# Optimization experiments

Hardware: AMD Instinct MI355X
Metric: run time of the kernel (lower is better)

Reference implementation:

```python
import jax, jax.numpy as jnp
import numpy as np

B, S1, S2 = 4, 2048, 2048
IN1, IN2 = 512, 512
KD, VD, H = 64, 64, 8


def setup_inputs() -> dict:
    key = jax.random.key(0)
    ks = jax.random.split(key, 7)
    x1 = jax.random.normal(ks[0], (B, S1, IN1), dtype=jnp.float32)
    x2 = jax.random.normal(ks[1], (B, S2, IN2), dtype=jnp.float32)
    # nn.Linear weights stored as [out, in]; kaiming-uniform-ish scale
    Wq = jax.random.normal(ks[2], (KD * H, IN1), dtype=jnp.float32) * (1.0 / np.sqrt(IN1))
    Wk = jax.random.normal(ks[3], (KD * H, IN2), dtype=jnp.float32) * (1.0 / np.sqrt(IN2))
    Wv = jax.random.normal(ks[4], (VD * H, IN2), dtype=jnp.float32) * (1.0 / np.sqrt(IN2))
    Wo = jax.random.normal(ks[5], (IN1, VD * H), dtype=jnp.float32) * (1.0 / np.sqrt(VD * H))
    bo = jax.random.normal(ks[6], (IN1,), dtype=jnp.float32) * 0.01
    return {"x1": x1, "x2": x2, "Wq": Wq, "Wk": Wk, "Wv": Wv, "Wo": Wo, "bo": bo}


def reference(x1, x2, Wq, Wk, Wv, Wo, bo):
    b, s1, _ = x1.shape
    s2 = x2.shape[1]
    # projections -> [B, H, S, D]
    q = (x1 @ Wq.T).reshape(b, s1, H, KD).transpose(0, 2, 1, 3)
    k = (x2 @ Wk.T).reshape(b, s2, H, KD).transpose(0, 2, 1, 3)
    v = (x2 @ Wv.T).reshape(b, s2, H, VD).transpose(0, 2, 1, 3)
    # scores [B, H, S1, S2]
    attn = jnp.einsum('bhqd,bhkd->bhqk', q, k) / jnp.sqrt(jnp.float32(KD))
    attn = jax.nn.softmax(attn, axis=-1)
    out = jnp.einsum('bhqk,bhkd->bhqd', attn, v)  # [B, H, S1, VD]
    out = out.transpose(0, 2, 1, 3).reshape(b, s1, H * VD)
    return out @ Wo.T + bo
```

## Files before the change

kernel.cpp:

```cpp
#include <hip/hip_runtime.h>
#include <stdint.h>

typedef __bf16 bf16;
typedef __bf16 bf16x8 __attribute__((ext_vector_type(8)));
typedef __bf16 bf16x4 __attribute__((ext_vector_type(4)));
typedef float f32x4 __attribute__((ext_vector_type(4)));

#define MFMA16x16x32(A, B, C) __builtin_amdgcn_mfma_f32_16x16x32_bf16((A), (B), (C), 0, 0, 0)

__device__ __forceinline__ void gload_lds16(const void* g, void* l) {
  __builtin_amdgcn_global_load_lds((const __attribute__((address_space(1))) void*)g,
                                   (__attribute__((address_space(3))) void*)l,
                                   16, 0, 0);
}

__device__ __forceinline__ float fexp2(float x) { return __builtin_amdgcn_exp2f(x); }

__device__ __forceinline__ bf16x8 cvt8(float4 a, float4 b) {
  bf16x8 o;
  o[0] = (bf16)a.x; o[1] = (bf16)a.y; o[2] = (bf16)a.z; o[3] = (bf16)a.w;
  o[4] = (bf16)b.x; o[5] = (bf16)b.y; o[6] = (bf16)b.z; o[7] = (bf16)b.w;
  return o;
}

__global__ void cast_x(const float* __restrict__ x1, const float* __restrict__ x2,
                       bf16* __restrict__ out) {
  const size_t i = ((size_t)blockIdx.x * blockDim.x + threadIdx.x) * 8;
  const float* src = (i < 4194304) ? x1 + i : x2 + (i - 4194304);
  float4 a = *reinterpret_cast<const float4*>(src);
  float4 b = *reinterpret_cast<const float4*>(src + 4);
  *reinterpret_cast<bf16x8*>(out + i) = cvt8(a, b);
}

template <int MODE>
__global__ __launch_bounds__(256, 4) void proj_kernel(
    const bf16* __restrict__ A0, const bf16* __restrict__ A1,
    const float* __restrict__ W0, const float* __restrict__ W1,
    const float* __restrict__ W2, void* __restrict__ C0, void* __restrict__ C1,
    void* __restrict__ C2, const float* __restrict__ bias) {
  __shared__ bf16 As[2][128 * 32];
  __shared__ bf16 Bs[2][64 * 32];
  const int tid = threadIdx.x;
  const int w = tid >> 6, l = tid & 63;
  const int wr = w >> 1, wc = w & 1;
  const int lr = l & 15, lg = l >> 4;
  const int bm = blockIdx.x, bn = blockIdx.y;
  const int K = 512;

  int sel = 0, wn = bn;
  const bf16* A;
  const float* Bf;
  if constexpr (MODE == 0) {
    sel = bn >> 3;
    wn = bn & 7;
    A = (sel == 0) ? A0 : A1;
    Bf = ((sel == 0) ? W0 : (sel == 1) ? W1 : W2) + (size_t)wn * 64 * K;
  } else {
    A = A0;
    Bf = W0 + (size_t)bn * 64 * K;
  }

  const int c_row = l >> 2;
  const int c_s = l & 3;
  const int sw = (c_s ^ (c_row & 3)) * 8;

  float4 lb[2][2];
  auto issue_B = [&](int t, int s) {
    const float* pb = Bf + (size_t)(w * 16 + c_row) * K + t * 32 + c_s * 8;
    lb[s][0] = *reinterpret_cast<const float4*>(pb);
    lb[s][1] = *reinterpret_cast<const float4*>(pb + 4);
  };
  auto commit_B = [&](int s, int bb) {
    *reinterpret_cast<bf16x8*>(&Bs[bb][w * 512 + c_row * 32 + sw]) = cvt8(lb[s][0], lb[s][1]);
  };
  auto issue_A = [&](int t, int bb) {
#pragma unroll
    for (int i = 0; i < 2; i++) {
      const int q = w + i * 4;
      gload_lds16(A + (size_t)(bm * 128 + q * 16 + c_row) * K + t * 32 + sw, &As[bb][q * 512]);
    }
  };

  f32x4 acc[4][2] = {};
  const int swz = (lr & 3) * 8;

  issue_B(0, 0);
  issue_A(0, 0);
  issue_B(1, 1);
  issue_A(1, 1);
  asm volatile("s_waitcnt vmcnt(4)" ::: "memory");
  commit_B(0, 0);
  __syncthreads();

  const int NT = K / 32;
  for (int t = 0; t < NT; t++) {
    const int cur = t & 1;
    if (t + 2 < NT) issue_B(t + 2, cur);

    bf16x8 a[4], b[2];
#pragma unroll
    for (int mi = 0; mi < 4; mi++)
      a[mi] = *reinterpret_cast<const bf16x8*>(
          &As[cur][(wr * 64 + mi * 16 + lr) * 32 + (lg * 8 ^ swz)]);
#pragma unroll
    for (int ni = 0; ni < 2; ni++)
      b[ni] = *reinterpret_cast<const bf16x8*>(
          &Bs[cur][(wc * 32 + ni * 16 + lr) * 32 + (lg * 8 ^ swz)]);
#pragma unroll
    for (int mi = 0; mi < 4; mi++)
#pragma unroll
      for (int ni = 0; ni < 2; ni++)
        acc[mi][ni] = MFMA16x16x32(a[mi], b[ni], acc[mi][ni]);

    if (t + 1 < NT) {
      if (t + 2 < NT) asm volatile("s_waitcnt vmcnt(2)" ::: "memory");
      else            asm volatile("s_waitcnt vmcnt(0)" ::: "memory");
      commit_B((t + 1) & 1, cur ^ 1);
      __syncthreads();
      if (t + 2 < NT) issue_A(t + 2, cur);
    }
  }

#pragma unroll
  for (int mi = 0; mi < 4; mi++) {
    const int m0 = bm * 128 + wr * 64 + mi * 16 + lg * 4;
#pragma unroll
    for (int ni = 0; ni < 2; ni++) {
      const int n = wc * 32 + ni * 16 + lr;
      if constexpr (MODE == 0) {
        const int gn = wn * 64 + n;
        if (sel < 2) {
          bf16* dst = (bf16*)((sel == 0) ? C0 : C1);
          const float scale = (sel == 0) ? 0.18033688011112f : 1.0f;
#pragma unroll
          for (int r = 0; r < 4; r++) {
            const int m = m0 + r;
            size_t d = (size_t)((m >> 11) * 8 + (gn >> 6)) * 131072 + (size_t)(m & 2047) * 64 + (gn & 63);
            dst[d] = (bf16)(acc[mi][ni][r] * scale);
          }
        } else {
          bf16x4 pv;
#pragma unroll
          for (int r = 0; r < 4; r++) pv[r] = (bf16)acc[mi][ni][r];
          size_t base = ((size_t)(m0 >> 11) * 512 + gn) * 2048 + (m0 & 2047);
          *reinterpret_cast<bf16x4*>((bf16*)C2 + base) = pv;
        }
      } else {
        const int gn = bn * 64 + n;
        const float bv = bias[gn];
#pragma unroll
        for (int r = 0; r < 4; r++)
          ((float*)C0)[(size_t)(m0 + r) * 512 + gn] = acc[mi][ni][r] + bv;
      }
    }
  }
}

__global__ __launch_bounds__(512, 1) void attn_kernel(
    const bf16* __restrict__ Q, const bf16* __restrict__ Kk,
    const bf16* __restrict__ Vt, bf16* __restrict__ AO) {
  __shared__ bf16 Kb2[2][64 * 64];
  __shared__ bf16 Vb2[2][64 * 64];
  __shared__ bf16 Ps[8][32 * 64];

  const int tid = threadIdx.x;
  const int w = tid >> 6, l = tid & 63;
  const int lr = l & 15, lg = l >> 4;

  const int lin = blockIdx.x;
  const int xcd = lin & 7;
  const int m = lin >> 3;
  const int bh = xcd * 4 + (m & 3);
  const int qb = m >> 2;
  const int b = bh >> 3, h = bh & 7;

  const bf16* Qb = Q + (size_t)bh * 131072;
  const bf16* Kb = Kk + (size_t)bh * 131072;
  const bf16* Vb = Vt + (size_t)bh * 131072;

  const int q0 = qb * 256 + w * 32;

  bf16x8 qf[2][2];
#pragma unroll
  for (int i = 0; i < 2; i++)
#pragma unroll
    for (int ks = 0; ks < 2; ks++)
      qf[i][ks] = *reinterpret_cast<const bf16x8*>(
          Qb + (size_t)(q0 + i * 16 + lr) * 64 + ks * 32 + lg * 8);

  const int crow = l >> 3;
  const int scol = ((l & 7) ^ crow) * 8;

  auto stage = [&](int kv0, int bb) {
    const int row = w * 8 + crow;
    gload_lds16(Kb + (size_t)(kv0 + row) * 64 + scol, &Kb2[bb][w * 512]);
    gload_lds16(Vb + (size_t)row * 2048 + kv0 + scol, &Vb2[bb][w * 512]);
  };

  f32x4 oacc[2][4] = {};
  float lsum[2] = {0.f, 0.f};
  const int sw8 = (lr & 7) * 8;

  stage(0, 0);
  asm volatile("s_waitcnt vmcnt(0)" ::: "memory");
  __syncthreads();

  for (int t = 0; t < 32; t++) {
    const int cur = t & 1;
    if (t < 31) stage((t + 1) * 64, cur ^ 1);

    bf16x8 kb[2][4];
#pragma unroll
    for (int ks = 0; ks < 2; ks++)
#pragma unroll
      for (int c = 0; c < 4; c++)
        kb[ks][c] = *reinterpret_cast<const bf16x8*>(
            &Kb2[cur][(c * 16 + lr) * 64 + ((ks * 32 + lg * 8) ^ sw8)]);

#pragma unroll
    for (int i = 0; i < 2; i++) {
      f32x4 st[4] = {};
#pragma unroll
      for (int ks = 0; ks < 2; ks++)
#pragma unroll
        for (int c = 0; c < 4; c++)
          st[c] = MFMA16x16x32(kb[ks][c], qf[i][ks], st[c]);
#pragma unroll
      for (int c = 0; c < 4; c++) {
        float e0 = fexp2(st[c][0]);
        float e1 = fexp2(st[c][1]);
        float e2 = fexp2(st[c][2]);
        float e3 = fexp2(st[c][3]);
        lsum[i] += (e0 + e1) + (e2 + e3);
        bf16x4 pk;
        pk[0] = (bf16)e0; pk[1] = (bf16)e1; pk[2] = (bf16)e2; pk[3] = (bf16)e3;
        *reinterpret_cast<bf16x4*>(
            &Ps[w][(i * 16 + lr) * 64 + ((c * 16 + lg * 4) ^ sw8)]) = pk;
      }
    }

    bf16x8 vb[2][4];
#pragma unroll
    for (int ks = 0; ks < 2; ks++)
#pragma unroll
      for (int c = 0; c < 4; c++)
        vb[ks][c] = *reinterpret_cast<const bf16x8*>(
            &Vb2[cur][(c * 16 + lr) * 64 + ((ks * 32 + lg * 8) ^ sw8)]);

#pragma unroll
    for (int i = 0; i < 2; i++)
#pragma unroll
      for (int ks = 0; ks < 2; ks++) {
        bf16x8 pa = *reinterpret_cast<const bf16x8*>(
            &Ps[w][(i * 16 + lr) * 64 + ((ks * 32 + lg * 8) ^ sw8)]);
#pragma unroll
        for (int c = 0; c < 4; c++)
          oacc[i][c] = MFMA16x16x32(pa, vb[ks][c], oacc[i][c]);
      }

    if (t < 31) asm volatile("s_waitcnt vmcnt(0)" ::: "memory");
    __syncthreads();
  }

#pragma unroll
  for (int i = 0; i < 2; i++) {
    lsum[i] += __shfl_xor(lsum[i], 16);
    lsum[i] += __shfl_xor(lsum[i], 32);
  }

#pragma unroll
  for (int i = 0; i < 2; i++) {
#pragma unroll
    for (int r = 0; r < 4; r++) {
      const float inv = 1.f / __shfl(lsum[i], lg * 4 + r);
      const int qrow = q0 + i * 16 + lg * 4 + r;
#pragma unroll
      for (int c = 0; c < 4; c++)
        AO[(size_t)(b * 2048 + qrow) * 512 + h * 64 + c * 16 + lr] = (bf16)(oacc[i][c][r] * inv);
    }
  }
}

extern "C" void kernel_launch(void* const* d_in, const int* in_sizes, int n_in,
                              void* d_out, int out_size, void* d_ws, size_t ws_size,
                              hipStream_t stream) {
  (void)in_sizes; (void)n_in; (void)out_size; (void)ws_size;
  const float* x1 = (const float*)d_in[0];
  const float* x2 = (const float*)d_in[1];
  const float* Wq = (const float*)d_in[2];
  const float* Wk = (const float*)d_in[3];
  const float* Wv = (const float*)d_in[4];
  const float* Wo = (const float*)d_in[5];
  const float* bo = (const float*)d_in[6];

  uint8_t* ws = (uint8_t*)d_ws;
  bf16* x1b = (bf16*)(ws + 0);
  bf16* x2b = (bf16*)(ws + 8388608);
  bf16* AO  = (bf16*)(ws + 0);
  bf16* Qws = (bf16*)(ws + 16777216);
  bf16* Kws = (bf16*)(ws + 25165824);
  bf16* Vtw = (bf16*)(ws + 33554432);

  cast_x<<<4096, 256, 0, stream>>>(x1, x2, x1b);

  proj_kernel<0><<<dim3(64, 24), 256, 0, stream>>>(x1b, x2b, Wq, Wk, Wv, Qws, Kws, Vtw, nullptr);

  attn_kernel<<<256, 512, 0, stream>>>(Qws, Kws, Vtw, AO);

  proj_kernel<1><<<dim3(64, 8), 256, 0, stream>>>(AO, nullptr, Wo, nullptr, nullptr, d_out, nullptr, nullptr, bo);
}
```

Baseline: 102.8 us.

## Triple-buffer GEMM/attention loads and split attention KV across wave pairs

The projection GEMM gets a third LDS buffer for A so A tiles are prefetched two iterations ahead, and __syncthreads is replaced by an explicit lgkmcnt wait plus raw s_barrier. The attention kernel also triple-buffers K/V and now gives each wave 64 query rows and half of each 64-wide KV tile. The two KV halves are combined at the end through an LDS reduction of partial outputs and row sums. This raises per-wave MFMA work per loaded Q/K fragment and deepens the prefetch, at the cost of more LDS, more registers, and an extra cross-wave reduction.

```diff
diff --git a/kernel.cpp b/kernel.cpp
--- a/kernel.cpp
+++ b/kernel.cpp
@@ -7,6 +7,7 @@
 typedef float f32x4 __attribute__((ext_vector_type(4)));
 
 #define MFMA16x16x32(A, B, C) __builtin_amdgcn_mfma_f32_16x16x32_bf16((A), (B), (C), 0, 0, 0)
+#define SBAR() do { __builtin_amdgcn_s_barrier(); __builtin_amdgcn_sched_barrier(0); } while (0)
 
 __device__ __forceinline__ void gload_lds16(const void* g, void* l) {
   __builtin_amdgcn_global_load_lds((const __attribute__((address_space(1))) void*)g,
@@ -38,7 +39,7 @@
     const float* __restrict__ W0, const float* __restrict__ W1,
     const float* __restrict__ W2, void* __restrict__ C0, void* __restrict__ C1,
     void* __restrict__ C2, const float* __restrict__ bias) {
-  __shared__ bf16 As[2][128 * 32];
+  __shared__ bf16 As[3][128 * 32];
   __shared__ bf16 Bs[2][64 * 32];
   const int tid = threadIdx.x;
   const int w = tid >> 6, l = tid & 63;
@@ -65,6 +66,13 @@
   const int sw = (c_s ^ (c_row & 3)) * 8;
 
   float4 lb[2][2];
+  auto issue_A = [&](int t, int bb) {
+#pragma unroll
+    for (int i = 0; i < 2; i++) {
+      const int q = w + i * 4;
+      gload_lds16(A + (size_t)(bm * 128 + q * 16 + c_row) * K + t * 32 + sw, &As[bb][q * 512]);
+    }
+  };
   auto issue_B = [&](int t, int s) {
     const float* pb = Bf + (size_t)(w * 16 + c_row) * K + t * 32 + c_s * 8;
     lb[s][0] = *reinterpret_cast<const float4*>(pb);
@@ -73,31 +81,23 @@
   auto commit_B = [&](int s, int bb) {
     *reinterpret_cast<bf16x8*>(&Bs[bb][w * 512 + c_row * 32 + sw]) = cvt8(lb[s][0], lb[s][1]);
   };
-  auto issue_A = [&](int t, int bb) {
-#pragma unroll
-    for (int i = 0; i < 2; i++) {
-      const int q = w + i * 4;
-      gload_lds16(A + (size_t)(bm * 128 + q * 16 + c_row) * K + t * 32 + sw, &As[bb][q * 512]);
-    }
-  };
 
   f32x4 acc[4][2] = {};
   const int swz = (lr & 3) * 8;
 
-  issue_B(0, 0);
-  issue_A(0, 0);
-  issue_B(1, 1);
-  issue_A(1, 1);
+  issue_A(0, 0); issue_B(0, 0);
+  issue_A(1, 1); issue_B(1, 1);
   asm volatile("s_waitcnt vmcnt(4)" ::: "memory");
   commit_B(0, 0);
-  __syncthreads();
-
-  const int NT = K / 32;
+  asm volatile("s_waitcnt lgkmcnt(0)" ::: "memory");
+  SBAR();
+
+  const int NT = 16;
   for (int t = 0; t < NT; t++) {
-    const int cur = t & 1;
-    if (t + 2 < NT) issue_B(t + 2, cur);
+    if (t + 2 < NT) { issue_A(t + 2, (t + 2) % 3); issue_B(t + 2, t & 1); }
 
     bf16x8 a[4], b[2];
+    const int cur = t % 3;
 #pragma unroll
     for (int mi = 0; mi < 4; mi++)
       a[mi] = *reinterpret_cast<const bf16x8*>(
@@ -105,7 +105,7 @@
 #pragma unroll
     for (int ni = 0; ni < 2; ni++)
       b[ni] = *reinterpret_cast<const bf16x8*>(
-          &Bs[cur][(wc * 32 + ni * 16 + lr) * 32 + (lg * 8 ^ swz)]);
+          &Bs[t & 1][(wc * 32 + ni * 16 + lr) * 32 + (lg * 8 ^ swz)]);
 #pragma unroll
     for (int mi = 0; mi < 4; mi++)
 #pragma unroll
@@ -113,11 +113,11 @@
         acc[mi][ni] = MFMA16x16x32(a[mi], b[ni], acc[mi][ni]);
 
     if (t + 1 < NT) {
-      if (t + 2 < NT) asm volatile("s_waitcnt vmcnt(2)" ::: "memory");
+      if (t + 2 < NT) asm volatile("s_waitcnt vmcnt(4)" ::: "memory");
       else            asm volatile("s_waitcnt vmcnt(0)" ::: "memory");
-      commit_B((t + 1) & 1, cur ^ 1);
-      __syncthreads();
-      if (t + 2 < NT) issue_A(t + 2, cur);
+      commit_B((t + 1) & 1, (t + 1) & 1);
+      asm volatile("s_waitcnt lgkmcnt(0)" ::: "memory");
+      SBAR();
     }
   }
 
@@ -159,13 +159,16 @@
 __global__ __launch_bounds__(512, 1) void attn_kernel(
     const bf16* __restrict__ Q, const bf16* __restrict__ Kk,
     const bf16* __restrict__ Vt, bf16* __restrict__ AO) {
-  __shared__ bf16 Kb2[2][64 * 64];
-  __shared__ bf16 Vb2[2][64 * 64];
-  __shared__ bf16 Ps[8][32 * 64];
+  __shared__ bf16 Kb2[3][64 * 64];
+  __shared__ bf16 Vb2[3][64 * 64];
+  __shared__ bf16 Ps[8][64 * 32];
+  __shared__ float Cb[4][64 * 64];
+  __shared__ float Ls2[4][64];
 
   const int tid = threadIdx.x;
   const int w = tid >> 6, l = tid & 63;
   const int lr = l & 15, lg = l >> 4;
+  const int qg = w & 3, kvh = w >> 2;
 
   const int lin = blockIdx.x;
   const int xcd = lin & 7;
@@ -178,11 +181,11 @@
   const bf16* Kb = Kk + (size_t)bh * 131072;
   const bf16* Vb = Vt + (size_t)bh * 131072;
 
-  const int q0 = qb * 256 + w * 32;
-
-  bf16x8 qf[2][2];
-#pragma unroll
-  for (int i = 0; i < 2; i++)
+  const int q0 = qb * 256 + qg * 64;
+
+  bf16x8 qf[4][2];
+#pragma unroll
+  for (int i = 0; i < 4; i++)
 #pragma unroll
     for (int ks = 0; ks < 2; ks++)
       qf[i][ks] = *reinterpret_cast<const bf16x8*>(
@@ -190,43 +193,44 @@
 
   const int crow = l >> 3;
   const int scol = ((l & 7) ^ crow) * 8;
-
   auto stage = [&](int kv0, int bb) {
     const int row = w * 8 + crow;
     gload_lds16(Kb + (size_t)(kv0 + row) * 64 + scol, &Kb2[bb][w * 512]);
     gload_lds16(Vb + (size_t)row * 2048 + kv0 + scol, &Vb2[bb][w * 512]);
   };
 
-  f32x4 oacc[2][4] = {};
-  float lsum[2] = {0.f, 0.f};
+  f32x4 oacc[4][4] = {};
+  float lsum[4] = {0.f, 0.f, 0.f, 0.f};
   const int sw8 = (lr & 7) * 8;
+  const int swp = (lr >> 2) & 3;
 
   stage(0, 0);
-  asm volatile("s_waitcnt vmcnt(0)" ::: "memory");
-  __syncthreads();
+  stage(64, 1);
+  asm volatile("s_waitcnt vmcnt(2)" ::: "memory");
+  SBAR();
 
   for (int t = 0; t < 32; t++) {
-    const int cur = t & 1;
-    if (t < 31) stage((t + 1) * 64, cur ^ 1);
-
-    bf16x8 kb[2][4];
+    const int cur = t % 3;
+    if (t + 2 < 32) stage((t + 2) * 64, (t + 2) % 3);
+
+    bf16x8 kb[2][2];
 #pragma unroll
     for (int ks = 0; ks < 2; ks++)
 #pragma unroll
-      for (int c = 0; c < 4; c++)
+      for (int c = 0; c < 2; c++)
         kb[ks][c] = *reinterpret_cast<const bf16x8*>(
-            &Kb2[cur][(c * 16 + lr) * 64 + ((ks * 32 + lg * 8) ^ sw8)]);
-
-#pragma unroll
-    for (int i = 0; i < 2; i++) {
-      f32x4 st[4] = {};
+            &Kb2[cur][(kvh * 32 + c * 16 + lr) * 64 + ((ks * 32 + lg * 8) ^ sw8)]);
+
+#pragma unroll
+    for (int i = 0; i < 4; i++) {
+      f32x4 st[2] = {};
 #pragma unroll
       for (int ks = 0; ks < 2; ks++)
 #pragma unroll
-        for (int c = 0; c < 4; c++)
+        for (int c = 0; c < 2; c++)
           st[c] = MFMA16x16x32(kb[ks][c], qf[i][ks], st[c]);
 #pragma unroll
-      for (int c = 0; c < 4; c++) {
+      for (int c = 0; c < 2; c++) {
         float e0 = fexp2(st[c][0]);
         float e1 = fexp2(st[c][1]);
         float e2 = fexp2(st[c][2]);
@@ -235,48 +239,69 @@
         bf16x4 pk;
         pk[0] = (bf16)e0; pk[1] = (bf16)e1; pk[2] = (bf16)e2; pk[3] = (bf16)e3;
         *reinterpret_cast<bf16x4*>(
-            &Ps[w][(i * 16 + lr) * 64 + ((c * 16 + lg * 4) ^ sw8)]) = pk;
+            &Ps[w][(i * 16 + lr) * 32 + ((c * 2 + (lg >> 1)) ^ swp) * 8 + (lg & 1) * 4]) = pk;
       }
     }
 
-    bf16x8 vb[2][4];
-#pragma unroll
-    for (int ks = 0; ks < 2; ks++)
+    bf16x8 vb[4];
+#pragma unroll
+    for (int c = 0; c < 4; c++)
+      vb[c] = *reinterpret_cast<const bf16x8*>(
+          &Vb2[cur][(c * 16 + lr) * 64 + ((kvh * 32 + lg * 8) ^ sw8)]);
+
+#pragma unroll
+    for (int i = 0; i < 4; i++) {
+      bf16x8 pa = *reinterpret_cast<const bf16x8*>(
+          &Ps[w][(i * 16 + lr) * 32 + (lg ^ swp) * 8]);
 #pragma unroll
       for (int c = 0; c < 4; c++)
-        vb[ks][c] = *reinterpret_cast<const bf16x8*>(
-            &Vb2[cur][(c * 16 + lr) * 64 + ((ks * 32 + lg * 8) ^ sw8)]);
-
-#pragma unroll
-    for (int i = 0; i < 2; i++)
-#pragma unroll
-      for (int ks = 0; ks < 2; ks++) {
-        bf16x8 pa = *reinterpret_cast<const bf16x8*>(
-            &Ps[w][(i * 16 + lr) * 64 + ((ks * 32 + lg * 8) ^ sw8)]);
-#pragma unroll
-        for (int c = 0; c < 4; c++)
-          oacc[i][c] = MFMA16x16x32(pa, vb[ks][c], oacc[i][c]);
-      }
-
-    if (t < 31) asm volatile("s_waitcnt vmcnt(0)" ::: "memory");
-    __syncthreads();
-  }
-
-#pragma unroll
-  for (int i = 0; i < 2; i++) {
+        oacc[i][c] = MFMA16x16x32(pa, vb[c], oacc[i][c]);
+    }
+
+    if (t < 30)       asm volatile("s_waitcnt vmcnt(2) lgkmcnt(0)" ::: "memory");
+    else if (t == 30) asm volatile("s_waitcnt vmcnt(0) lgkmcnt(0)" ::: "memory");
+    if (t < 31) SBAR();
+  }
+
+#pragma unroll
+  for (int i = 0; i < 4; i++) {
     lsum[i] += __shfl_xor(lsum[i], 16);
     lsum[i] += __shfl_xor(lsum[i], 32);
   }
 
-#pragma unroll
-  for (int i = 0; i < 2; i++) {
-#pragma unroll
-    for (int r = 0; r < 4; r++) {
-      const float inv = 1.f / __shfl(lsum[i], lg * 4 + r);
-      const int qrow = q0 + i * 16 + lg * 4 + r;
+  if (kvh == 1) {
+#pragma unroll
+    for (int i = 0; i < 4; i++)
 #pragma unroll
       for (int c = 0; c < 4; c++)
-        AO[(size_t)(b * 2048 + qrow) * 512 + h * 64 + c * 16 + lr] = (bf16)(oacc[i][c][r] * inv);
+        *reinterpret_cast<f32x4*>(
+            &Cb[qg][(c * 16 + lr) * 64 + ((i * 4 + lg) ^ (lr & 3)) * 4]) = oacc[i][c];
+    if (lg == 0) {
+#pragma unroll
+      for (int i = 0; i < 4; i++) Ls2[qg][i * 16 + lr] = lsum[i];
+    }
+  }
+  __syncthreads();
+  if (kvh == 0) {
+#pragma unroll
+    for (int i = 0; i < 4; i++) {
+      lsum[i] += Ls2[qg][i * 16 + lr];
+#pragma unroll
+      for (int c = 0; c < 4; c++)
+        oacc[i][c] += *reinterpret_cast<const f32x4*>(
+            &Cb[qg][(c * 16 + lr) * 64 + ((i * 4 + lg) ^ (lr & 3)) * 4]);
+    }
+#pragma unroll
+    for (int i = 0; i < 4; i++) {
+#pragma unroll
+      for (int r = 0; r < 4; r++) {
+        const float inv = 1.f / __shfl(lsum[i], lg * 4 + r);
+        const int qrow = q0 + i * 16 + lg * 4 + r;
+#pragma unroll
+        for (int c = 0; c < 4; c++)
+          AO[(size_t)(b * 2048 + qrow) * 512 + h * 64 + c * 16 + lr] =
+              (bf16)(oacc[i][c][r] * inv);
+      }
     }
   }
 }
```

Result: slower. 106.3 us (+3.4%).

## Triple-buffer projection A tiles and load attention K/V directly from global

Applied to the files above, without the earlier changes.

The projection GEMM moves to a three-stage LDS ring for the A operand, issuing A and B loads two tiles ahead and replacing __syncthreads with a raw barrier plus explicit waitcnts. The attention kernel drops its shared K/V staging and block barriers. Each wave now reads K and V fragments straight from global/L2 into registers, with K loads software-pipelined one tile ahead. This removes LDS traffic and per-iteration block synchronisation, but each of the 8 waves now fetches K/V redundantly from cache and V reads are strided and unhidden.

```diff
diff --git a/kernel.cpp b/kernel.cpp
--- a/kernel.cpp
+++ b/kernel.cpp
@@ -7,6 +7,7 @@
 typedef float f32x4 __attribute__((ext_vector_type(4)));
 
 #define MFMA16x16x32(A, B, C) __builtin_amdgcn_mfma_f32_16x16x32_bf16((A), (B), (C), 0, 0, 0)
+#define SBAR() do { __builtin_amdgcn_s_barrier(); __builtin_amdgcn_sched_barrier(0); } while (0)
 
 __device__ __forceinline__ void gload_lds16(const void* g, void* l) {
   __builtin_amdgcn_global_load_lds((const __attribute__((address_space(1))) void*)g,
@@ -38,7 +39,7 @@
     const float* __restrict__ W0, const float* __restrict__ W1,
     const float* __restrict__ W2, void* __restrict__ C0, void* __restrict__ C1,
     void* __restrict__ C2, const float* __restrict__ bias) {
-  __shared__ bf16 As[2][128 * 32];
+  __shared__ bf16 As[3][128 * 32];
   __shared__ bf16 Bs[2][64 * 32];
   const int tid = threadIdx.x;
   const int w = tid >> 6, l = tid & 63;
@@ -65,6 +66,13 @@
   const int sw = (c_s ^ (c_row & 3)) * 8;
 
   float4 lb[2][2];
+  auto issue_A = [&](int t, int bb) {
+#pragma unroll
+    for (int i = 0; i < 2; i++) {
+      const int q = w + i * 4;
+      gload_lds16(A + (size_t)(bm * 128 + q * 16 + c_row) * K + t * 32 + sw, &As[bb][q * 512]);
+    }
+  };
   auto issue_B = [&](int t, int s) {
     const float* pb = Bf + (size_t)(w * 16 + c_row) * K + t * 32 + c_s * 8;
     lb[s][0] = *reinterpret_cast<const float4*>(pb);
@@ -73,31 +81,23 @@
   auto commit_B = [&](int s, int bb) {
     *reinterpret_cast<bf16x8*>(&Bs[bb][w * 512 + c_row * 32 + sw]) = cvt8(lb[s][0], lb[s][1]);
   };
-  auto issue_A = [&](int t, int bb) {
-#pragma unroll
-    for (int i = 0; i < 2; i++) {
-      const int q = w + i * 4;
-      gload_lds16(A + (size_t)(bm * 128 + q * 16 + c_row) * K + t * 32 + sw, &As[bb][q * 512]);
-    }
-  };
 
   f32x4 acc[4][2] = {};
   const int swz = (lr & 3) * 8;
 
-  issue_B(0, 0);
-  issue_A(0, 0);
-  issue_B(1, 1);
-  issue_A(1, 1);
+  issue_A(0, 0); issue_B(0, 0);
+  issue_A(1, 1); issue_B(1, 1);
   asm volatile("s_waitcnt vmcnt(4)" ::: "memory");
   commit_B(0, 0);
-  __syncthreads();
-
-  const int NT = K / 32;
+  asm volatile("s_waitcnt lgkmcnt(0)" ::: "memory");
+  SBAR();
+
+  const int NT = 16;
   for (int t = 0; t < NT; t++) {
-    const int cur = t & 1;
-    if (t + 2 < NT) issue_B(t + 2, cur);
+    if (t + 2 < NT) { issue_A(t + 2, (t + 2) % 3); issue_B(t + 2, t & 1); }
 
     bf16x8 a[4], b[2];
+    const int cur = t % 3;
 #pragma unroll
     for (int mi = 0; mi < 4; mi++)
       a[mi] = *reinterpret_cast<const bf16x8*>(
@@ -105,7 +105,7 @@
 #pragma unroll
     for (int ni = 0; ni < 2; ni++)
       b[ni] = *reinterpret_cast<const bf16x8*>(
-          &Bs[cur][(wc * 32 + ni * 16 + lr) * 32 + (lg * 8 ^ swz)]);
+          &Bs[t & 1][(wc * 32 + ni * 16 + lr) * 32 + (lg * 8 ^ swz)]);
 #pragma unroll
     for (int mi = 0; mi < 4; mi++)
 #pragma unroll
@@ -113,11 +113,11 @@
         acc[mi][ni] = MFMA16x16x32(a[mi], b[ni], acc[mi][ni]);
 
     if (t + 1 < NT) {
-      if (t + 2 < NT) asm volatile("s_waitcnt vmcnt(2)" ::: "memory");
+      if (t + 2 < NT) asm volatile("s_waitcnt vmcnt(4)" ::: "memory");
       else            asm volatile("s_waitcnt vmcnt(0)" ::: "memory");
-      commit_B((t + 1) & 1, cur ^ 1);
-      __syncthreads();
-      if (t + 2 < NT) issue_A(t + 2, cur);
+      commit_B((t + 1) & 1, (t + 1) & 1);
+      asm volatile("s_waitcnt lgkmcnt(0)" ::: "memory");
+      SBAR();
     }
   }
 
@@ -159,8 +159,6 @@
 __global__ __launch_bounds__(512, 1) void attn_kernel(
     const bf16* __restrict__ Q, const bf16* __restrict__ Kk,
     const bf16* __restrict__ Vt, bf16* __restrict__ AO) {
-  __shared__ bf16 Kb2[2][64 * 64];
-  __shared__ bf16 Vb2[2][64 * 64];
   __shared__ bf16 Ps[8][32 * 64];
 
   const int tid = threadIdx.x;
@@ -188,35 +186,20 @@
       qf[i][ks] = *reinterpret_cast<const bf16x8*>(
           Qb + (size_t)(q0 + i * 16 + lr) * 64 + ks * 32 + lg * 8);
 
-  const int crow = l >> 3;
-  const int scol = ((l & 7) ^ crow) * 8;
-
-  auto stage = [&](int kv0, int bb) {
-    const int row = w * 8 + crow;
-    gload_lds16(Kb + (size_t)(kv0 + row) * 64 + scol, &Kb2[bb][w * 512]);
-    gload_lds16(Vb + (size_t)row * 2048 + kv0 + scol, &Vb2[bb][w * 512]);
-  };
-
   f32x4 oacc[2][4] = {};
   float lsum[2] = {0.f, 0.f};
   const int sw8 = (lr & 7) * 8;
 
-  stage(0, 0);
-  asm volatile("s_waitcnt vmcnt(0)" ::: "memory");
-  __syncthreads();
-
-  for (int t = 0; t < 32; t++) {
-    const int cur = t & 1;
-    if (t < 31) stage((t + 1) * 64, cur ^ 1);
-
-    bf16x8 kb[2][4];
+  auto loadK = [&](int kv0, bf16x8 (&kb)[2][4]) {
 #pragma unroll
     for (int ks = 0; ks < 2; ks++)
 #pragma unroll
       for (int c = 0; c < 4; c++)
         kb[ks][c] = *reinterpret_cast<const bf16x8*>(
-            &Kb2[cur][(c * 16 + lr) * 64 + ((ks * 32 + lg * 8) ^ sw8)]);
-
+            Kb + (size_t)(kv0 + c * 16 + lr) * 64 + ks * 32 + lg * 8);
+  };
+
+  auto body = [&](int kv0, bf16x8 (&kb)[2][4]) {
 #pragma unroll
     for (int i = 0; i < 2; i++) {
       f32x4 st[4] = {};
@@ -245,7 +228,7 @@
 #pragma unroll
       for (int c = 0; c < 4; c++)
         vb[ks][c] = *reinterpret_cast<const bf16x8*>(
-            &Vb2[cur][(c * 16 + lr) * 64 + ((ks * 32 + lg * 8) ^ sw8)]);
+            Vb + (size_t)(c * 16 + lr) * 2048 + kv0 + ks * 32 + lg * 8);
 
 #pragma unroll
     for (int i = 0; i < 2; i++)
@@ -257,9 +240,15 @@
         for (int c = 0; c < 4; c++)
           oacc[i][c] = MFMA16x16x32(pa, vb[ks][c], oacc[i][c]);
       }
-
-    if (t < 31) asm volatile("s_waitcnt vmcnt(0)" ::: "memory");
-    __syncthreads();
+  };
+
+  bf16x8 kbA[2][4], kbB[2][4];
+  loadK(0, kbA);
+  for (int t = 0; t < 32; t += 2) {
+    loadK((t + 1) * 64, kbB);
+    body(t * 64, kbA);
+    if (t + 2 < 32) loadK((t + 2) * 64, kbA);
+    body((t + 1) * 64, kbB);
   }
 
 #pragma unroll
```

New measurement: 170.0 us. 65.5% more time.
